# Kernel tuning notes

Measured on AMD Instinct MI355X. Metric: run time of the kernel, lower is better.

The kernel has to match this reference:

```python
import math
import jax, jax.numpy as jnp
from jax import lax
import numpy as np

LN_EPS = 1e-5
K = 3          # deform-conv kernel size
PAD = 1        # 'same' padding so offset map matches output resolution


def setup_inputs() -> dict:
    key = jax.random.key(0)
    ks = jax.random.split(key, 6)
    B, C, H, W, Co = 4, 256, 64, 64, 256
    x = jax.random.normal(ks[0], (B, C, H, W), jnp.float32)
    dwc_w = jax.random.normal(ks[1], (C, 1, K, K), jnp.float32) * 0.02
    ln_w = jnp.ones((C,), jnp.float32)
    ln_b = jnp.zeros((C,), jnp.float32)
    fcd_w = jax.random.normal(ks[2], (1, C, 1, 1), jnp.float32) * 0.02
    fca_w = jax.random.normal(ks[3], (1, C, 1, 1), jnp.float32) * 0.02
    fan_in = C * K * K
    dconv_w = jax.random.normal(ks[4], (Co, C, K, K), jnp.float32) / math.sqrt(fan_in)
    dconv_b = jnp.zeros((Co,), jnp.float32)
    return dict(x=x, dwc_w=dwc_w, ln_w=ln_w, ln_b=ln_b,
                fcd_w=fcd_w, fca_w=fca_w, dconv_w=dconv_w, dconv_b=dconv_b)


def _bilinear_sample(x, py, px):
    # x: [B,C,H,W]; py/px: [B,KK,H,W] float sample positions (zero-padded border)
    B, C, H, W = x.shape
    y0 = jnp.floor(py); x0 = jnp.floor(px)
    y1 = y0 + 1.0;      x1 = x0 + 1.0
    wy1 = py - y0; wy0 = 1.0 - wy1
    wx1 = px - x0; wx0 = 1.0 - wx1

    def gather(yy, xx):
        valid = ((yy >= 0) & (yy < H) & (xx >= 0) & (xx < W)).astype(x.dtype)
        iy = jnp.clip(yy, 0, H - 1).astype(jnp.int32)
        ix = jnp.clip(xx, 0, W - 1).astype(jnp.int32)
        # per-batch fancy gather -> [B,C,KK,H,W]
        v = jax.vmap(lambda img, a, b: img[:, a, b])(x, iy, ix)
        return v * valid[:, None]

    return (gather(y0, x0) * (wy0 * wx0)[:, None]
          + gather(y0, x1) * (wy0 * wx1)[:, None]
          + gather(y1, x0) * (wy1 * wx0)[:, None]
          + gather(y1, x1) * (wy1 * wx1)[:, None])


def reference(x, dwc_w, ln_w, ln_b, fcd_w, fca_w, dconv_w, dconv_b):
    B, C, H, W = x.shape
    KK = K * K
    # --- offset branch ---
    h = lax.conv_general_dilated(x, dwc_w, (1, 1), ((1, 1), (1, 1)),
                                 dimension_numbers=('NCHW', 'OIHW', 'NCHW'),
                                 feature_group_count=C)
    mu = h.mean(axis=1, keepdims=True)
    var = h.var(axis=1, keepdims=True)
    h = (h - mu) * lax.rsqrt(var + LN_EPS)
    h = h * ln_w[None, :, None, None] + ln_b[None, :, None, None]
    h = jax.nn.relu(h)
    r = jax.nn.relu(jnp.einsum('bchw,oc->bohw', h, fcd_w[:, :, 0, 0]))      # [B,1,H,W]
    t = jnp.einsum('bchw,oc->bohw', h, fca_w[:, :, 0, 0])
    theta = (t / (1.0 + jnp.abs(t))) * (math.pi / 180.0)                     # softsign * pi/180
    ox = r * jnp.cos(theta)
    oy = r * jnp.sin(theta)
    # torch code: offsets = cat([ox tiled KK, oy tiled KK], dim=1) -> [B,2KK,H,W]
    off = jnp.concatenate([jnp.tile(ox, (1, KK, 1, 1)), jnp.tile(oy, (1, KK, 1, 1))], axis=1)
    # torchvision DeformConv2d convention: channel 2k = dy, channel 2k+1 = dx
    dy = off[:, 0::2]   # [B,KK,H,W]
    dx = off[:, 1::2]
    # --- deformable sampling ---
    ky = jnp.repeat(jnp.arange(K), K).astype(x.dtype)   # kernel row per tap
    kx = jnp.tile(jnp.arange(K), K).astype(x.dtype)     # kernel col per tap
    py = (jnp.arange(H, dtype=x.dtype) - PAD)[None, None, :, None] + ky[None, :, None, None] + dy
    px = (jnp.arange(W, dtype=x.dtype) - PAD)[None, None, None, :] + kx[None, :, None, None] + dx
    sampled = _bilinear_sample(x, py, px)               # [B,C,KK,H,W]
    Co = dconv_w.shape[0]
    out = jnp.einsum('bckhw,ock->bohw', sampled, dconv_w.reshape(Co, C, KK))
    return out + dconv_b[None, :, None, None]
```

## Files before the change

### kernel.cpp

```cpp
#include <hip/hip_runtime.h>
#include <hip/hip_bf16.h>

#define B_   4
#define C_   256
#define CO_  256
#define H_   64
#define W_   64
#define HW_  4096

typedef __attribute__((ext_vector_type(8))) short short8;
typedef __attribute__((ext_vector_type(4))) float f32x4;
typedef __attribute__((ext_vector_type(2))) float f32x2;

static __device__ __forceinline__ unsigned short f2bf(float f) {
    unsigned u = __builtin_bit_cast(unsigned, f);
    unsigned r = (u + 0x7fffu + ((u >> 16) & 1u)) >> 16;
    return (unsigned short)r;
}
static __device__ __forceinline__ f32x2 pk_mul(f32x2 a, f32x2 b) {
    f32x2 d; asm("v_pk_mul_f32 %0, %1, %2" : "=v"(d) : "v"(a), "v"(b)); return d;
}
static __device__ __forceinline__ f32x2 pk_fma(f32x2 a, f32x2 b, f32x2 c) {
    f32x2 d; asm("v_pk_fma_f32 %0, %1, %2, %3" : "=v"(d) : "v"(a), "v"(b), "v"(c)); return d;
}
static __device__ __forceinline__ f32x2 pk_add(f32x2 a, f32x2 b) {
    f32x2 d; asm("v_pk_add_f32 %0, %1, %2" : "=v"(d) : "v"(a), "v"(b)); return d;
}
static __device__ __forceinline__ unsigned cvtpk(float a, float b) {
    unsigned r; asm("v_cvt_pk_bf16_f32 %0, %1, %2" : "=v"(r) : "v"(a), "v"(b)); return r;
}
static __device__ __forceinline__ f32x2 unpack_bf2(unsigned d) {
    f32x2 v;
    v.x = __builtin_bit_cast(float, d << 16);
    v.y = __builtin_bit_cast(float, d & 0xffff0000u);
    return v;
}

__global__ void k_transpose(const float* __restrict__ x, unsigned short* __restrict__ xT)
{
    __shared__ float t[32][132];
    int bid = blockIdx.x;
    int b   = bid >> 8;
    int rem = bid & 255;
    int hwT = rem >> 1, cT = rem & 1;
    int hw0 = hwT * 32, c0 = cT * 128;
    int tid = threadIdx.x;
    const float* src = x + (size_t)b * C_ * HW_;
    {
        int hw4 = (tid & 7) << 2;
        int cr  = tid >> 3;
#pragma unroll
        for (int it = 0; it < 4; ++it) {
            int c = cr + it * 32;
            f32x4 v = *(const f32x4*)(src + (size_t)(c0 + c) * HW_ + hw0 + hw4);
            t[hw4 + 0][c] = v.x;
            t[hw4 + 1][c] = v.y;
            t[hw4 + 2][c] = v.z;
            t[hw4 + 3][c] = v.w;
        }
    }
    __syncthreads();
    {
        int c8  = (tid & 15) << 3;
        int hwr = tid >> 4;
        unsigned short* dst = xT + (size_t)(((b << 12) + hw0) * 256) + c0 + c8;
#pragma unroll
        for (int it = 0; it < 2; ++it) {
            int hw = hwr + it * 16;
            f32x4 va = *(const f32x4*)&t[hw][c8];
            f32x4 vb = *(const f32x4*)&t[hw][c8 + 4];
            uint4 u;
            u.x = cvtpk(va.x, va.y);
            u.y = cvtpk(va.z, va.w);
            u.z = cvtpk(vb.x, vb.y);
            u.w = cvtpk(vb.z, vb.w);
            *(uint4*)(dst + (size_t)hw * 256) = u;
        }
    }
}

__global__ void k_packB(const float* __restrict__ w, unsigned short* __restrict__ Bt,
                        const float* __restrict__ dwc_w, float* __restrict__ dwcT)
{
    int bid = blockIdx.x;
    int tid = threadIdx.x;
    if (bid < 9) dwcT[bid * 256 + tid] = dwc_w[tid * 9 + bid];
    int e = bid * 256 + tid;
    int j   = e & 7;
    int l4  = (e >> 3) & 3;
    int l15 = (e >> 5) & 15;
    int ks  = (e >> 9) & 7;
    int og  = (e >> 12) & 15;
    int k   = e >> 16;
    int o = og * 16 + l15;
    int c = ks * 32 + l4 * 8 + j;
    Bt[e] = f2bf(w[(o * C_ + c) * 9 + k]);
}

__global__ void k_offsets(const unsigned short* __restrict__ xT,
                          const float* __restrict__ dwcT,
                          const float* __restrict__ ln_w,
                          const float* __restrict__ ln_b,
                          const float* __restrict__ fcd_w,
                          const float* __restrict__ fca_w,
                          float* __restrict__ OX, float* __restrict__ OY)
{
    int tid = threadIdx.x;
    int bi = blockIdx.x;
    int g = ((bi & 7) << 6) | (bi >> 3);
    int p0 = g << 5;
    int b = p0 >> 12;
    int y = (p0 >> 6) & 63;
    int xh = p0 & 63;
    int gpos = tid >> 4;
    int csub = tid & 15;
    int ch0 = csub << 4;
    const unsigned short* xb = xT + (size_t)b * HW_ * C_;

    f32x2 acc2[8];
#pragma unroll
    for (int i = 0; i < 8; ++i) { acc2[i].x = 0.f; acc2[i].y = 0.f; }
#pragma unroll
    for (int j = 0; j < 9; ++j) {
        int gy = y + j / 3 - 1, gx = xh + gpos + j % 3 - 1;
        if (gy >= 0 && gy < H_ && gx >= 0 && gx < W_) {
            const unsigned short* p = xb + (size_t)((gy << 6) + gx) * 256 + ch0;
            short8 rlo = *(const short8*)(p);
            short8 rhi = *(const short8*)(p + 8);
            const float* wrow = dwcT + j * 256 + ch0;
#pragma unroll
            for (int q = 0; q < 4; ++q) {
                f32x4 wv = *(const f32x4*)(wrow + q * 4);
                f32x2 w01v; w01v.x = wv.x; w01v.y = wv.y;
                f32x2 w23v; w23v.x = wv.z; w23v.y = wv.w;
                unsigned lo = (q < 2) ? ((unsigned*)&rlo)[q * 2] : ((unsigned*)&rhi)[(q - 2) * 2];
                unsigned hi = (q < 2) ? ((unsigned*)&rlo)[q * 2 + 1] : ((unsigned*)&rhi)[(q - 2) * 2 + 1];
                acc2[q * 2 + 0] = pk_fma(unpack_bf2(lo), w01v, acc2[q * 2 + 0]);
                acc2[q * 2 + 1] = pk_fma(unpack_bf2(hi), w23v, acc2[q * 2 + 1]);
            }
        }
    }
    f32x2 sum2, sq2;
    sum2.x = 0.f; sum2.y = 0.f; sq2.x = 0.f; sq2.y = 0.f;
#pragma unroll
    for (int i = 0; i < 8; ++i) {
        sum2 = pk_add(sum2, acc2[i]);
        sq2  = pk_fma(acc2[i], acc2[i], sq2);
    }
    float s1 = sum2.x + sum2.y, s2 = sq2.x + sq2.y;
#pragma unroll
    for (int m = 1; m <= 8; m <<= 1) {
        s1 += __shfl_xor(s1, m);
        s2 += __shfl_xor(s2, m);
    }
    float mu  = s1 * (1.f / 256.f);
    float var = s2 * (1.f / 256.f) - mu * mu;
    float rs  = rsqrtf(var + 1e-5f);
    float d1 = 0.f, d2 = 0.f;
#pragma unroll
    for (int q = 0; q < 4; ++q) {
        f32x4 lwv = *(const f32x4*)(ln_w  + ch0 + q * 4);
        f32x4 lbv = *(const f32x4*)(ln_b  + ch0 + q * 4);
        f32x4 fdv = *(const f32x4*)(fcd_w + ch0 + q * 4);
        f32x4 fav = *(const f32x4*)(fca_w + ch0 + q * 4);
#pragma unroll
        for (int i = 0; i < 4; ++i) {
            float av = (i & 1) ? acc2[q * 2 + (i >> 1)].y : acc2[q * 2 + (i >> 1)].x;
            float hn = (av - mu) * rs * lwv[i] + lbv[i];
            hn = fmaxf(hn, 0.f);
            d1 = fmaf(hn, fdv[i], d1);
            d2 = fmaf(hn, fav[i], d2);
        }
    }
#pragma unroll
    for (int m = 1; m <= 8; m <<= 1) {
        d1 += __shfl_xor(d1, m);
        d2 += __shfl_xor(d2, m);
    }
    if (csub == 0) {
        float r0 = fmaxf(d1, 0.f);
        float theta = d2 / (1.f + fabsf(d2)) * 0.017453292519943295f;
        int pos = p0 + gpos;
        OX[pos] = r0 * cosf(theta);
        OY[pos] = r0 * sinf(theta);
    }
}

__launch_bounds__(512, 4)
__global__ void k_main(const unsigned short* __restrict__ xT,
                       const float* __restrict__ OX, const float* __restrict__ OY,
                       const unsigned short* __restrict__ Bt,
                       const float* __restrict__ bias,
                       float* __restrict__ out)
{
    __shared__ __align__(16) unsigned char smem[65536];

    int tid = threadIdx.x;
    int bi = blockIdx.x;
    int g = ((bi & 7) << 6) | (bi >> 3);
    int tile = g >> 1;
    int n0g = g & 1;
    int b = tile >> 6;
    int y = tile & 63;

    int lane = tid & 63, wid = tid >> 6;
    int l15 = lane & 15, l4 = lane >> 4;

    f32x4 acc[4];
#pragma unroll
    for (int m = 0; m < 4; ++m) {
        acc[m].x = 0.f; acc[m].y = 0.f; acc[m].z = 0.f; acc[m].w = 0.f;
    }

    int gpos = tid >> 3;
    unsigned csub16 = ((unsigned)tid & 7u) << 4;
    const char* xbB = (const char*)(xT + (size_t)b * HW_ * C_);
    const unsigned short* bwave = Bt + (unsigned)(n0g * 8 + wid) * 4096u
                                     + (unsigned)(l15 * 32 + l4 * 8);
    unsigned rowb = (unsigned)gpos * 512u;
    unsigned swzcol = csub16 ^ (((unsigned)gpos & 7u) << 4);
    float ox = OX[(tile << 6) + gpos], oy = OY[(tile << 6) + gpos];

#define GADDR(k)                                                                  \
        int ky = (k) / 3, kx = (k) - ky * 3;                                      \
        float dyv = ((k) <= 4) ? ox : oy;                                         \
        float dxv = ((k) <= 3) ? ox : oy;                                         \
        float py = (float)(y - 1 + ky) + dyv;                                     \
        float px = (float)(gpos - 1 + kx) + dxv;                                  \
        float y0f = floorf(py), x0f = floorf(px);                                 \
        int y0 = (int)y0f, x0 = (int)x0f;                                         \
        int y1 = y0 + 1, x1 = x0 + 1;                                             \
        float wy1 = py - y0f, wy0 = 1.f - wy1;                                    \
        float wx1 = px - x0f, wx0 = 1.f - wx1;                                    \
        float vy0 = (y0 >= 0 && y0 < H_) ? 1.f : 0.f;                             \
        float vy1 = (y1 >= 0 && y1 < H_) ? 1.f : 0.f;                             \
        float vx0 = (x0 >= 0 && x0 < W_) ? 1.f : 0.f;                             \
        float vx1 = (x1 >= 0 && x1 < W_) ? 1.f : 0.f;                             \
        w00 = wy0 * wx0 * vy0 * vx0; w01 = wy0 * wx1 * vy0 * vx1;                 \
        w10 = wy1 * wx0 * vy1 * vx0; w11 = wy1 * wx1 * vy1 * vx1;                 \
        int y0c = min(max(y0, 0), H_ - 1), y1c = min(max(y1, 0), H_ - 1);         \
        int x0c = min(max(x0, 0), W_ - 1), x1c = min(max(x1, 0), W_ - 1);         \
        o00 = (unsigned)((y0c << 6) + x0c) * 512u + csub16;                       \
        o01 = (unsigned)((y0c << 6) + x1c) * 512u + csub16;                       \
        o10 = (unsigned)((y1c << 6) + x0c) * 512u + csub16;                       \
        o11 = (unsigned)((y1c << 6) + x1c) * 512u + csub16;

#define GATHER_TAP(k, buf)                                                        \
    {   unsigned o00, o01, o10, o11;                                              \
        float w00, w01, w10, w11;                                                 \
        GADDR(k);                                                                 \
        f32x2 W00, W01, W10, W11;                                                 \
        W00.x = w00; W00.y = w00; W01.x = w01; W01.y = w01;                       \
        W10.x = w10; W10.y = w10; W11.x = w11; W11.y = w11;                       \
        unsigned wb = (unsigned)(buf) * 32768u + rowb + swzcol;                   \
        _Pragma("unroll")                                                         \
        for (int cq = 0; cq < 4; ++cq) {                                          \
            short8 r00 = *(const short8*)(xbB + o00 + cq * 128);                  \
            short8 r01 = *(const short8*)(xbB + o01 + cq * 128);                  \
            short8 r10 = *(const short8*)(xbB + o10 + cq * 128);                  \
            short8 r11 = *(const short8*)(xbB + o11 + cq * 128);                  \
            uint4 pkv;                                                            \
            _Pragma("unroll")                                                     \
            for (int dw = 0; dw < 4; ++dw) {                                      \
                f32x2 a2 = pk_mul(unpack_bf2(((unsigned*)&r00)[dw]), W00);        \
                a2 = pk_fma(unpack_bf2(((unsigned*)&r01)[dw]), W01, a2);          \
                a2 = pk_fma(unpack_bf2(((unsigned*)&r10)[dw]), W10, a2);          \
                a2 = pk_fma(unpack_bf2(((unsigned*)&r11)[dw]), W11, a2);          \
                ((unsigned*)&pkv)[dw] = cvtpk(a2.x, a2.y);                        \
            }                                                                     \
            *(uint4*)(smem + wb + cq * 128) = pkv;                                \
        }                                                                         \
    }

    GATHER_TAP(0, 0);
    __syncthreads();

#pragma unroll
    for (int k = 0; k < 9; ++k) {
        int t = k & 1;
        {
            const unsigned short* bk = bwave + (unsigned)k * 65536u;
            unsigned abase = (unsigned)t * 32768u;
#pragma unroll
            for (int ks = 0; ks < 8; ++ks) {
                short8 bf = *(const short8*)(bk + ks * 512);
                unsigned coff = (unsigned)(ks * 64 + (l4 << 4)) ^ (((unsigned)l15 & 7u) << 4);
#pragma unroll
                for (int mf = 0; mf < 4; ++mf) {
                    short8 a = *(const short8*)(smem + abase +
                                 (unsigned)(mf * 16 + l15) * 512u + coff);
                    acc[mf] = __builtin_amdgcn_mfma_f32_16x16x32_bf16(a, bf, acc[mf], 0, 0, 0);
                }
            }
        }
        if (k < 8) {
            GATHER_TAP(k + 1, t ^ 1);
        }
        __syncthreads();
    }

    float* epi = (float*)smem;
#pragma unroll
    for (int mf = 0; mf < 4; ++mf)
#pragma unroll
        for (int i = 0; i < 4; ++i) {
            int row = mf * 16 + l4 * 4 + i;
            int col = wid * 16 + l15;
            epi[row * 133 + col] = acc[mf][i];
        }
    __syncthreads();
    int o  = tid >> 2;
    int wq = (tid & 3) << 4;
    float bv = bias[n0g * 128 + o];
    float* orow = out + (size_t)(((b * CO_ + n0g * 128 + o) * H_ + y) * W_) + wq;
#pragma unroll
    for (int j = 0; j < 16; j += 4) {
        f32x4 v;
        v.x = epi[(wq + j + 0) * 133 + o] + bv;
        v.y = epi[(wq + j + 1) * 133 + o] + bv;
        v.z = epi[(wq + j + 2) * 133 + o] + bv;
        v.w = epi[(wq + j + 3) * 133 + o] + bv;
        *(f32x4*)(orow + j) = v;
    }
}

extern "C" void kernel_launch(void* const* d_in, const int* in_sizes, int n_in,
                              void* d_out, int out_size, void* d_ws, size_t ws_size,
                              hipStream_t stream) {
    const float* x      = (const float*)d_in[0];
    const float* dwc_w  = (const float*)d_in[1];
    const float* ln_w   = (const float*)d_in[2];
    const float* ln_b   = (const float*)d_in[3];
    const float* fcd_w  = (const float*)d_in[4];
    const float* fca_w  = (const float*)d_in[5];
    const float* dconv_w= (const float*)d_in[6];
    const float* dconv_b= (const float*)d_in[7];
    float* out = (float*)d_out;

    unsigned char* ws = (unsigned char*)d_ws;
    unsigned short* xT = (unsigned short*)(ws);
    unsigned short* Bt = (unsigned short*)(ws + 8388608);
    float* dwcT        = (float*)(ws + 9568256);
    float* OX          = (float*)(ws + 9577472);
    float* OY          = (float*)(ws + 9643008);

    k_transpose<<<1024, 256, 0, stream>>>(x, xT);
    k_packB<<<2304, 256, 0, stream>>>(dconv_w, Bt, dwc_w, dwcT);
    k_offsets<<<512, 512, 0, stream>>>(xT, dwcT, ln_w, ln_b, fcd_w, fca_w, OX, OY);
    k_main<<<512, 512, 0, stream>>>(xT, OX, OY, Bt, dconv_b, out);
}
```

Baseline: 76.39 us.

## Split tap gather into channel halves, halve LDS, fuse prep kernels, direct epilogue

The main kernel now stages each tap's gathered A tile in two 128-channel halves using a 32 KB LDS buffer instead of two full 32 KB buffers. Gather of one half is interleaved with MFMA on the other half, and the XOR swizzle is widened to 16 slots. Halving LDS is meant to raise occupancy and improve overlap, at the cost of two barriers per tap instead of one. The LDS-transposed epilogue is replaced by direct stores from the accumulators, and the transpose and weight-pack kernels are merged into one launch to cut launch overhead.

```diff
diff --git a/kernel.cpp b/kernel.cpp
--- a/kernel.cpp
+++ b/kernel.cpp
@@ -36,65 +36,64 @@
     return v;
 }
 
-__global__ void k_transpose(const float* __restrict__ x, unsigned short* __restrict__ xT)
-{
-    __shared__ float t[32][132];
-    int bid = blockIdx.x;
-    int b   = bid >> 8;
-    int rem = bid & 255;
-    int hwT = rem >> 1, cT = rem & 1;
-    int hw0 = hwT * 32, c0 = cT * 128;
-    int tid = threadIdx.x;
-    const float* src = x + (size_t)b * C_ * HW_;
-    {
-        int hw4 = (tid & 7) << 2;
-        int cr  = tid >> 3;
-#pragma unroll
-        for (int it = 0; it < 4; ++it) {
-            int c = cr + it * 32;
-            f32x4 v = *(const f32x4*)(src + (size_t)(c0 + c) * HW_ + hw0 + hw4);
-            t[hw4 + 0][c] = v.x;
-            t[hw4 + 1][c] = v.y;
-            t[hw4 + 2][c] = v.z;
-            t[hw4 + 3][c] = v.w;
-        }
-    }
-    __syncthreads();
-    {
-        int c8  = (tid & 15) << 3;
-        int hwr = tid >> 4;
-        unsigned short* dst = xT + (size_t)(((b << 12) + hw0) * 256) + c0 + c8;
-#pragma unroll
-        for (int it = 0; it < 2; ++it) {
-            int hw = hwr + it * 16;
-            f32x4 va = *(const f32x4*)&t[hw][c8];
-            f32x4 vb = *(const f32x4*)&t[hw][c8 + 4];
-            uint4 u;
-            u.x = cvtpk(va.x, va.y);
-            u.y = cvtpk(va.z, va.w);
-            u.z = cvtpk(vb.x, vb.y);
-            u.w = cvtpk(vb.z, vb.w);
-            *(uint4*)(dst + (size_t)hw * 256) = u;
-        }
-    }
-}
-
-__global__ void k_packB(const float* __restrict__ w, unsigned short* __restrict__ Bt,
-                        const float* __restrict__ dwc_w, float* __restrict__ dwcT)
+__global__ void k_pre(const float* __restrict__ x, unsigned short* __restrict__ xT,
+                      const float* __restrict__ w, unsigned short* __restrict__ Bt,
+                      const float* __restrict__ dwc_w, float* __restrict__ dwcT)
 {
     int bid = blockIdx.x;
     int tid = threadIdx.x;
-    if (bid < 9) dwcT[bid * 256 + tid] = dwc_w[tid * 9 + bid];
-    int e = bid * 256 + tid;
-    int j   = e & 7;
-    int l4  = (e >> 3) & 3;
-    int l15 = (e >> 5) & 15;
-    int ks  = (e >> 9) & 7;
-    int og  = (e >> 12) & 15;
-    int k   = e >> 16;
-    int o = og * 16 + l15;
-    int c = ks * 32 + l4 * 8 + j;
-    Bt[e] = f2bf(w[(o * C_ + c) * 9 + k]);
+    if (bid < 1024) {
+        __shared__ float t[32][132];
+        int b   = bid >> 8;
+        int rem = bid & 255;
+        int hwT = rem >> 1, cT = rem & 1;
+        int hw0 = hwT * 32, c0 = cT * 128;
+        const float* src = x + (size_t)b * C_ * HW_;
+        {
+            int hw4 = (tid & 7) << 2;
+            int cr  = tid >> 3;
+#pragma unroll
+            for (int it = 0; it < 4; ++it) {
+                int c = cr + it * 32;
+                f32x4 v = *(const f32x4*)(src + (size_t)(c0 + c) * HW_ + hw0 + hw4);
+                t[hw4 + 0][c] = v.x;
+                t[hw4 + 1][c] = v.y;
+                t[hw4 + 2][c] = v.z;
+                t[hw4 + 3][c] = v.w;
+            }
+        }
+        __syncthreads();
+        {
+            int c8  = (tid & 15) << 3;
+            int hwr = tid >> 4;
+            unsigned short* dst = xT + (size_t)(((b << 12) + hw0) * 256) + c0 + c8;
+#pragma unroll
+            for (int it = 0; it < 2; ++it) {
+                int hw = hwr + it * 16;
+                f32x4 va = *(const f32x4*)&t[hw][c8];
+                f32x4 vb = *(const f32x4*)&t[hw][c8 + 4];
+                uint4 u;
+                u.x = cvtpk(va.x, va.y);
+                u.y = cvtpk(va.z, va.w);
+                u.z = cvtpk(vb.x, vb.y);
+                u.w = cvtpk(vb.z, vb.w);
+                *(uint4*)(dst + (size_t)hw * 256) = u;
+            }
+        }
+    } else {
+        int pb = bid - 1024;
+        if (pb < 9) dwcT[pb * 256 + tid] = dwc_w[tid * 9 + pb];
+        int e = pb * 256 + tid;
+        int j   = e & 7;
+        int l4  = (e >> 3) & 3;
+        int l15 = (e >> 5) & 15;
+        int ks  = (e >> 9) & 7;
+        int og  = (e >> 12) & 15;
+        int k   = e >> 16;
+        int o = og * 16 + l15;
+        int c = ks * 32 + l4 * 8 + j;
+        Bt[e] = f2bf(w[(o * C_ + c) * 9 + k]);
+    }
 }
 
 __global__ void k_offsets(const unsigned short* __restrict__ xT,
@@ -193,7 +192,7 @@
                        const float* __restrict__ bias,
                        float* __restrict__ out)
 {
-    __shared__ __align__(16) unsigned char smem[65536];
+    __shared__ __align__(16) unsigned char smem[32768];
 
     int tid = threadIdx.x;
     int bi = blockIdx.x;
@@ -213,16 +212,20 @@
     }
 
     int gpos = tid >> 3;
-    unsigned csub16 = ((unsigned)tid & 7u) << 4;
+    unsigned csub = (unsigned)tid & 7u;
     const char* xbB = (const char*)(xT + (size_t)b * HW_ * C_);
     const unsigned short* bwave = Bt + (unsigned)(n0g * 8 + wid) * 4096u
                                      + (unsigned)(l15 * 32 + l4 * 8);
-    unsigned rowb = (unsigned)gpos * 512u;
-    unsigned swzcol = csub16 ^ (((unsigned)gpos & 7u) << 4);
+    unsigned rowb = (unsigned)gpos * 256u;
+    unsigned wsl0 = (csub ^ ((unsigned)gpos & 15u)) << 4;
+    unsigned wsl1 = ((8u + csub) ^ ((unsigned)gpos & 15u)) << 4;
     float ox = OX[(tile << 6) + gpos], oy = OY[(tile << 6) + gpos];
 
+    unsigned o00, o01, o10, o11;
+    f32x2 W00, W01, W10, W11;
+
 #define GADDR(k)                                                                  \
-        int ky = (k) / 3, kx = (k) - ky * 3;                                      \
+    {   int ky = (k) / 3, kx = (k) - ky * 3;                                      \
         float dyv = ((k) <= 4) ? ox : oy;                                         \
         float dxv = ((k) <= 3) ? ox : oy;                                         \
         float py = (float)(y - 1 + ky) + dyv;                                     \
@@ -236,29 +239,27 @@
         float vy1 = (y1 >= 0 && y1 < H_) ? 1.f : 0.f;                             \
         float vx0 = (x0 >= 0 && x0 < W_) ? 1.f : 0.f;                             \
         float vx1 = (x1 >= 0 && x1 < W_) ? 1.f : 0.f;                             \
-        w00 = wy0 * wx0 * vy0 * vx0; w01 = wy0 * wx1 * vy0 * vx1;                 \
-        w10 = wy1 * wx0 * vy1 * vx0; w11 = wy1 * wx1 * vy1 * vx1;                 \
+        float w00 = wy0 * wx0 * vy0 * vx0, w01 = wy0 * wx1 * vy0 * vx1;           \
+        float w10 = wy1 * wx0 * vy1 * vx0, w11 = wy1 * wx1 * vy1 * vx1;           \
+        W00.x = w00; W00.y = w00; W01.x = w01; W01.y = w01;                       \
+        W10.x = w10; W10.y = w10; W11.x = w11; W11.y = w11;                       \
         int y0c = min(max(y0, 0), H_ - 1), y1c = min(max(y1, 0), H_ - 1);         \
         int x0c = min(max(x0, 0), W_ - 1), x1c = min(max(x1, 0), W_ - 1);         \
-        o00 = (unsigned)((y0c << 6) + x0c) * 512u + csub16;                       \
-        o01 = (unsigned)((y0c << 6) + x1c) * 512u + csub16;                       \
-        o10 = (unsigned)((y1c << 6) + x0c) * 512u + csub16;                       \
-        o11 = (unsigned)((y1c << 6) + x1c) * 512u + csub16;
-
-#define GATHER_TAP(k, buf)                                                        \
-    {   unsigned o00, o01, o10, o11;                                              \
-        float w00, w01, w10, w11;                                                 \
-        GADDR(k);                                                                 \
-        f32x2 W00, W01, W10, W11;                                                 \
-        W00.x = w00; W00.y = w00; W01.x = w01; W01.y = w01;                       \
-        W10.x = w10; W10.y = w10; W11.x = w11; W11.y = w11;                       \
-        unsigned wb = (unsigned)(buf) * 32768u + rowb + swzcol;                   \
-        _Pragma("unroll")                                                         \
-        for (int cq = 0; cq < 4; ++cq) {                                          \
-            short8 r00 = *(const short8*)(xbB + o00 + cq * 128);                  \
-            short8 r01 = *(const short8*)(xbB + o01 + cq * 128);                  \
-            short8 r10 = *(const short8*)(xbB + o10 + cq * 128);                  \
-            short8 r11 = *(const short8*)(xbB + o11 + cq * 128);                  \
+        unsigned cb = csub << 4;                                                  \
+        o00 = (unsigned)((y0c << 6) + x0c) * 512u + cb;                           \
+        o01 = (unsigned)((y0c << 6) + x1c) * 512u + cb;                           \
+        o10 = (unsigned)((y1c << 6) + x0c) * 512u + cb;                           \
+        o11 = (unsigned)((y1c << 6) + x1c) * 512u + cb;                           \
+    }
+
+#define GATHER_HALF(h, hbase)                                                     \
+    {   _Pragma("unroll")                                                         \
+        for (int cq2 = 0; cq2 < 2; ++cq2) {                                       \
+            unsigned gb = (unsigned)(h) * 256u + (unsigned)cq2 * 128u;            \
+            short8 r00 = *(const short8*)(xbB + o00 + gb);                        \
+            short8 r01 = *(const short8*)(xbB + o01 + gb);                        \
+            short8 r10 = *(const short8*)(xbB + o10 + gb);                        \
+            short8 r11 = *(const short8*)(xbB + o11 + gb);                        \
             uint4 pkv;                                                            \
             _Pragma("unroll")                                                     \
             for (int dw = 0; dw < 4; ++dw) {                                      \
@@ -268,59 +269,54 @@
                 a2 = pk_fma(unpack_bf2(((unsigned*)&r11)[dw]), W11, a2);          \
                 ((unsigned*)&pkv)[dw] = cvtpk(a2.x, a2.y);                        \
             }                                                                     \
-            *(uint4*)(smem + wb + cq * 128) = pkv;                                \
+            *(uint4*)(smem + (hbase) + rowb + (cq2 ? wsl1 : wsl0)) = pkv;         \
         }                                                                         \
     }
 
-    GATHER_TAP(0, 0);
+#define MFMA_HALF(k, h, hbase)                                                    \
+    {   const unsigned short* bk = bwave + (unsigned)(k) * 65536u;                \
+        _Pragma("unroll")                                                         \
+        for (int ks2 = 0; ks2 < 4; ++ks2) {                                       \
+            int ks = (h) * 4 + ks2;                                               \
+            short8 bf = *(const short8*)(bk + ks * 512);                          \
+            unsigned sl = ((unsigned)(ks2 * 4 + l4) ^ (unsigned)l15) << 4;        \
+            _Pragma("unroll")                                                     \
+            for (int mf = 0; mf < 4; ++mf) {                                      \
+                unsigned row = (unsigned)(mf * 16 + l15);                         \
+                short8 a = *(const short8*)(smem + (hbase) + row * 256u + sl);    \
+                acc[mf] = __builtin_amdgcn_mfma_f32_16x16x32_bf16(a, bf, acc[mf], 0, 0, 0); \
+            }                                                                     \
+        }                                                                         \
+    }
+
+    GADDR(0);
+    GATHER_HALF(0, 0u);
     __syncthreads();
 
 #pragma unroll
     for (int k = 0; k < 9; ++k) {
-        int t = k & 1;
-        {
-            const unsigned short* bk = bwave + (unsigned)k * 65536u;
-            unsigned abase = (unsigned)t * 32768u;
-#pragma unroll
-            for (int ks = 0; ks < 8; ++ks) {
-                short8 bf = *(const short8*)(bk + ks * 512);
-                unsigned coff = (unsigned)(ks * 64 + (l4 << 4)) ^ (((unsigned)l15 & 7u) << 4);
-#pragma unroll
-                for (int mf = 0; mf < 4; ++mf) {
-                    short8 a = *(const short8*)(smem + abase +
-                                 (unsigned)(mf * 16 + l15) * 512u + coff);
-                    acc[mf] = __builtin_amdgcn_mfma_f32_16x16x32_bf16(a, bf, acc[mf], 0, 0, 0);
-                }
-            }
-        }
+        GATHER_HALF(1, 16384u);
+        MFMA_HALF(k, 0, 0u);
+        __syncthreads();
         if (k < 8) {
-            GATHER_TAP(k + 1, t ^ 1);
-        }
+            GADDR(k + 1);
+            GATHER_HALF(0, 0u);
+        }
+        MFMA_HALF(k, 1, 16384u);
         __syncthreads();
     }
 
-    float* epi = (float*)smem;
-#pragma unroll
-    for (int mf = 0; mf < 4; ++mf)
-#pragma unroll
-        for (int i = 0; i < 4; ++i) {
-            int row = mf * 16 + l4 * 4 + i;
-            int col = wid * 16 + l15;
-            epi[row * 133 + col] = acc[mf][i];
-        }
-    __syncthreads();
-    int o  = tid >> 2;
-    int wq = (tid & 3) << 4;
-    float bv = bias[n0g * 128 + o];
-    float* orow = out + (size_t)(((b * CO_ + n0g * 128 + o) * H_ + y) * W_) + wq;
-#pragma unroll
-    for (int j = 0; j < 16; j += 4) {
+    int col = n0g * 128 + wid * 16 + l15;
+    float bv = bias[col];
+    float* obase = out + ((size_t)(b * CO_ + col)) * HW_ + (y << 6);
+#pragma unroll
+    for (int mf = 0; mf < 4; ++mf) {
         f32x4 v;
-        v.x = epi[(wq + j + 0) * 133 + o] + bv;
-        v.y = epi[(wq + j + 1) * 133 + o] + bv;
-        v.z = epi[(wq + j + 2) * 133 + o] + bv;
-        v.w = epi[(wq + j + 3) * 133 + o] + bv;
-        *(f32x4*)(orow + j) = v;
+        v.x = acc[mf].x + bv;
+        v.y = acc[mf].y + bv;
+        v.z = acc[mf].z + bv;
+        v.w = acc[mf].w + bv;
+        *(f32x4*)(obase + mf * 16 + l4 * 4) = v;
     }
 }
 
@@ -344,8 +340,7 @@
     float* OX          = (float*)(ws + 9577472);
     float* OY          = (float*)(ws + 9643008);
 
-    k_transpose<<<1024, 256, 0, stream>>>(x, xT);
-    k_packB<<<2304, 256, 0, stream>>>(dconv_w, Bt, dwc_w, dwcT);
+    k_pre<<<3328, 256, 0, stream>>>(x, xT, dconv_w, Bt, dwc_w, dwcT);
     k_offsets<<<512, 512, 0, stream>>>(xT, dwcT, ln_w, ln_b, fcd_w, fca_w, OX, OY);
     k_main<<<512, 512, 0, stream>>>(xT, OX, OY, Bt, dconv_b, out);
 }
```

Result: faster. 73.49 us (-3.8%).
